# Optimization experiments

Measured on AMD Instinct MI355X. Metric: run time of the kernel, lower is better.

## Reference

```python
import jax, jax.numpy as jnp
import numpy as np

GAMMAS = (0.001, 0.01, 0.1, 1.0, 10.0, 100.0, 1000.0)
EPS = 1e-30


def setup_inputs() -> dict:
    key = jax.random.key(0)
    k1, k2 = jax.random.split(key)
    x = jax.random.normal(k1, (8192, 128), dtype=jnp.float32)
    y = jax.random.normal(k2, (8192, 128), dtype=jnp.float32)
    return {"x": x, "y": y}


def _cdist_sq(x1, x2):
    # squared Euclidean distance matrix, clamped at 1e-30 (matches my_cdist)
    x1_norm = jnp.sum(x1 * x1, axis=-1, keepdims=True)          # [N,1]
    x2_norm = jnp.sum(x2 * x2, axis=-1, keepdims=True)          # [M,1]
    d = x1_norm + x2_norm.T - 2.0 * (x1 @ x2.T)                 # [N,M]
    return jnp.maximum(d, EPS)


def _gaussian_kernel_mean(x, y):
    d = _cdist_sq(x, y)
    # sum over 7 bandwidths, fused into one pass conceptually
    k = sum(jnp.exp(d * (-g)) for g in GAMMAS)
    return jnp.mean(k)


def reference(x, y):
    kxx = _gaussian_kernel_mean(x, x)
    kyy = _gaussian_kernel_mean(y, y)
    kxy = _gaussian_kernel_mean(x, y)
    return kxx + kyy - 2.0 * kxy
```

## Files before the change

kernel.cpp:

```cpp
#include <hip/hip_runtime.h>


#define N_PTS 8192
#define D 128
#define TILES 64
#define TRI 2080
#define NBLK (2 * TRI + TILES * TILES)

typedef __attribute__((ext_vector_type(8))) short bf16x8;
typedef __attribute__((ext_vector_type(8))) unsigned short u16x8;
typedef __attribute__((ext_vector_type(4))) float f32x4;

__device__ __forceinline__ unsigned short f2bf(float a) {
  unsigned u = __float_as_uint(a);
  return (unsigned short)((u + 0x7FFFu + ((u >> 16) & 1u)) >> 16);
}
__device__ __forceinline__ float bf2f(unsigned short b) {
  return __uint_as_float(((unsigned)b) << 16);
}

__global__ __launch_bounds__(256) void norms_kernel(const float* __restrict__ x,
                                                    const float* __restrict__ y,
                                                    float* __restrict__ nx,
                                                    float* __restrict__ ny) {
  int tid = threadIdx.x;
  int g = tid & 3;
  int row = ((int)blockIdx.x & 127) * 64 + (tid >> 2);
  int arr = (int)blockIdx.x >> 7;
  const float* src = arr ? y : x;
  const float4* p = (const float4*)(src + (size_t)row * D) + g;
  float s = 0.f;
  #pragma unroll
  for (int i = 0; i < 8; i++) {
    float4 v = p[i * 4];
    s += v.x * v.x + v.y * v.y + v.z * v.z + v.w * v.w;
  }
  s += __shfl_xor(s, 1);
  s += __shfl_xor(s, 2);
  if (g == 0) (arr ? ny : nx)[row] = s;
}

__global__ __launch_bounds__(256) void convert_kernel(const float* __restrict__ x,
                                                      const float* __restrict__ y,
                                                      unsigned short* __restrict__ xf,
                                                      unsigned short* __restrict__ yf) {
  __shared__ float lds[4][16][132];
  int tid = threadIdx.x;
  int lane = tid & 63, wv = tid >> 6;
  int grp = (int)blockIdx.x * 4 + wv;
  int arr = grp >> 9;
  int rowgrp = grp & 511;
  const float* src = (arr ? y : x) + (size_t)rowgrp * 16 * D;
  unsigned short* dst = (arr ? yf : xf) + (size_t)rowgrp * 4096;

  #pragma unroll
  for (int it = 0; it < 8; it++) {
    int slot = it * 64 + lane;
    int row = slot >> 5, f4 = slot & 31;
    float4 v = *(const float4*)(src + row * D + f4 * 4);
    *(float4*)&lds[wv][row][f4 * 4] = v;
  }
  __syncthreads();

  int row = lane & 15, koct = lane >> 4;
  #pragma unroll
  for (int ks = 0; ks < 8; ks++) {
    int kp = ks * 32 + koct * 8;
    int kf = kp & 127;
    bool ishi = kp < 128;
    float v[8];
    *(float4*)&v[0] = *(const float4*)&lds[wv][row][kf];
    *(float4*)&v[4] = *(const float4*)&lds[wv][row][kf + 4];
    u16x8 o;
    #pragma unroll
    for (int j = 0; j < 8; j++) {
      unsigned short h = f2bf(v[j]);
      o[j] = ishi ? h : f2bf(v[j] - bf2f(h));
    }
    *(u16x8*)(dst + ks * 512 + lane * 8) = o;
  }
}

__global__ __launch_bounds__(256) void mmd_frag_kernel(const unsigned short* __restrict__ xf,
                                                       const unsigned short* __restrict__ yf,
                                                       const float* __restrict__ nx,
                                                       const float* __restrict__ ny,
                                                       double* __restrict__ acc_out) {
  __shared__ double red[256];
  int bid = blockIdx.x;
  const unsigned short *Af, *Bf;
  const float *nA, *nB;
  float w;
  int ib, jb;
  bool isdiag = false;
  if (bid < 2 * TRI) {
    int t = (bid < TRI) ? bid : bid - TRI;
    int r = 0;
    while (t >= TILES - r) { t -= TILES - r; r++; }
    ib = r; jb = r + t;
    if (bid < TRI) { Af = xf; Bf = xf; nA = nx; nB = nx; }
    else           { Af = yf; Bf = yf; nA = ny; nB = ny; }
    isdiag = (ib == jb);
    w = isdiag ? 1.0f : 2.0f;
  } else {
    int t = bid - 2 * TRI;
    ib = t >> 6; jb = t & 63;
    Af = xf; Bf = yf; nA = nx; nB = ny;
    w = -2.0f;
  }

  int tid = threadIdx.x;
  int lane = tid & 63;
  int wv = tid >> 6, wm = wv >> 1, wn = wv & 1;
  int r16 = lane & 15, g4 = lane >> 4;

  const char* Ab = (const char*)Af + (size_t)(ib * 8 + wm * 4) * 8192 + lane * 16;
  const char* Bb = (const char*)Bf + (size_t)(jb * 8 + wn * 4) * 8192 + lane * 16;

  f32x4 acc[4][4];
  #pragma unroll
  for (int m = 0; m < 4; m++)
    #pragma unroll
    for (int n = 0; n < 4; n++) acc[m][n] = (f32x4){0.f, 0.f, 0.f, 0.f};

  #pragma unroll
  for (int ks = 0; ks < 8; ks++) {
    bf16x8 af[4], bfr[4];
    #pragma unroll
    for (int m = 0; m < 4; m++)
      af[m] = *(const bf16x8*)(Ab + m * 8192 + ks * 1024);
    #pragma unroll
    for (int n = 0; n < 4; n++)
      bfr[n] = *(const bf16x8*)(Bb + n * 8192 + ks * 1024);
    #pragma unroll
    for (int m = 0; m < 4; m++)
      #pragma unroll
      for (int n = 0; n < 4; n++)
        acc[m][n] = __builtin_amdgcn_mfma_f32_16x16x32_bf16(af[m], bfr[n], acc[m][n], 0, 0, 0);
  }

  const float* nArow = nA + ib * 128;
  const float* nBrow = nB + jb * 128;
  float nb4[4];
  #pragma unroll
  for (int n = 0; n < 4; n++) nb4[n] = nBrow[wn * 64 + n * 16 + r16];

  float lsum = 0.f;
  #pragma unroll
  for (int m = 0; m < 4; m++) {
    float na4[4];
    #pragma unroll
    for (int r = 0; r < 4; r++) na4[r] = nArow[wm * 64 + m * 16 + g4 * 4 + r];
    float dv[4][4];
    float dmin = 3.0e38f;
    #pragma unroll
    for (int n = 0; n < 4; n++) {
      #pragma unroll
      for (int r = 0; r < 4; r++) {
        float dd = fmaf(-2.f, acc[m][n][r], na4[r] + nb4[n]);
        dd = fmaxf(dd, 1e-30f);
        int rl = wm * 64 + m * 16 + g4 * 4 + r;
        int cl = wn * 64 + n * 16 + r16;
        if (isdiag && rl == cl) dd = 1e30f;
        dv[n][r] = dd;
        dmin = fminf(dmin, dd);
      }
    }
    if (__all(dmin > 110.f)) {
      #pragma unroll
      for (int n = 0; n < 4; n++)
        #pragma unroll
        for (int r = 0; r < 4; r++) {
          float dd = dv[n][r];
          lsum += __expf(dd * -0.001f);
          lsum += __expf(dd * -0.01f);
          lsum += __expf(dd * -0.1f);
        }
    } else {
      #pragma unroll
      for (int n = 0; n < 4; n++)
        #pragma unroll
        for (int r = 0; r < 4; r++) {
          float dd = dv[n][r];
          lsum += __expf(dd * -0.001f);
          lsum += __expf(dd * -0.01f);
          lsum += __expf(dd * -0.1f);
          lsum += __expf(dd * -1.0f);
          lsum += __expf(dd * -10.0f);
          lsum += __expf(dd * -100.0f);
          lsum += __expf(dd * -1000.0f);
        }
    }
  }

  red[tid] = (double)lsum * (double)w;
  __syncthreads();
  #pragma unroll
  for (int s = 128; s > 0; s >>= 1) {
    if (tid < s) red[tid] += red[tid + s];
    __syncthreads();
  }
  if (tid == 0) atomicAdd(acc_out, red[0]);
}

__global__ __launch_bounds__(256) void mmd_fallback_kernel(const float* __restrict__ X,
                                                           const float* __restrict__ Y,
                                                           const float* __restrict__ nx,
                                                           const float* __restrict__ ny,
                                                           double* __restrict__ acc_out) {
  __shared__ unsigned short As[128 * 64];
  __shared__ unsigned short Bs[128 * 64];
  __shared__ double red[256];
  int bid = blockIdx.x;
  const float *A, *B, *nA, *nB;
  float w;
  int ib, jb;
  bool isdiag = false;
  if (bid < 2 * TRI) {
    int t = (bid < TRI) ? bid : bid - TRI;
    int r = 0;
    while (t >= TILES - r) { t -= TILES - r; r++; }
    ib = r; jb = r + t;
    if (bid < TRI) { A = X; B = X; nA = nx; nB = nx; }
    else           { A = Y; B = Y; nA = ny; nB = ny; }
    isdiag = (ib == jb);
    w = isdiag ? 1.0f : 2.0f;
  } else {
    int t = bid - 2 * TRI;
    ib = t >> 6; jb = t & 63;
    A = X; B = Y; nA = nx; nB = ny;
    w = -2.0f;
  }
  int tid = threadIdx.x;
  int lane = tid & 63;
  int wv = tid >> 6, wm = wv >> 1, wn = wv & 1;
  int r16 = lane & 15, g4 = lane >> 4;
  const float* Ab = A + (size_t)ib * 128 * D;
  const float* Bb = B + (size_t)jb * 128 * D;
  f32x4 acc[4][4];
  #pragma unroll
  for (int m = 0; m < 4; m++)
    #pragma unroll
    for (int n = 0; n < 4; n++) acc[m][n] = (f32x4){0.f, 0.f, 0.f, 0.f};
  #pragma unroll 1
  for (int kc = 0; kc < 4; kc++) {
    int k0f = (kc & 1) * 64;
    bool ishi = (kc < 2);
    __syncthreads();
    #pragma unroll
    for (int s = 0; s < 4; s++) {
      int slot = tid + s * 256;
      int row = slot >> 3;
      int k2 = (slot & 7) * 8;
      const float* pa = Ab + row * D + k0f + k2;
      const float* pb = Bb + row * D + k0f + k2;
      float4 a0 = *(const float4*)pa;
      float4 a1 = *(const float4*)(pa + 4);
      float4 b0 = *(const float4*)pb;
      float4 b1 = *(const float4*)(pb + 4);
      float av[8] = {a0.x, a0.y, a0.z, a0.w, a1.x, a1.y, a1.z, a1.w};
      float bv[8] = {b0.x, b0.y, b0.z, b0.w, b1.x, b1.y, b1.z, b1.w};
      u16x8 ua, ub;
      #pragma unroll
      for (int j = 0; j < 8; j++) {
        unsigned short ha = f2bf(av[j]);
        unsigned short hb = f2bf(bv[j]);
        if (ishi) { ua[j] = (short)ha; ub[j] = (short)hb; }
        else {
          ua[j] = f2bf(av[j] - bf2f(ha));
          ub[j] = f2bf(bv[j] - bf2f(hb));
        }
      }
      int boff = row * 128 + ((k2 * 2) ^ ((row & 7) << 4));
      *(u16x8*)((char*)As + boff) = ua;
      *(u16x8*)((char*)Bs + boff) = ub;
    }
    __syncthreads();
    #pragma unroll
    for (int ks = 0; ks < 2; ks++) {
      bf16x8 af[4], bfr[4];
      int kb = ks * 64 + g4 * 16;
      #pragma unroll
      for (int m = 0; m < 4; m++) {
        int row = wm * 64 + m * 16 + r16;
        af[m] = *(const bf16x8*)((const char*)As + row * 128 + (kb ^ ((row & 7) << 4)));
      }
      #pragma unroll
      for (int n = 0; n < 4; n++) {
        int row = wn * 64 + n * 16 + r16;
        bfr[n] = *(const bf16x8*)((const char*)Bs + row * 128 + (kb ^ ((row & 7) << 4)));
      }
      #pragma unroll
      for (int m = 0; m < 4; m++)
        #pragma unroll
        for (int n = 0; n < 4; n++)
          acc[m][n] = __builtin_amdgcn_mfma_f32_16x16x32_bf16(af[m], bfr[n], acc[m][n], 0, 0, 0);
    }
  }
  const float* nArow = nA + ib * 128;
  const float* nBrow = nB + jb * 128;
  float nb4[4];
  #pragma unroll
  for (int n = 0; n < 4; n++) nb4[n] = nBrow[wn * 64 + n * 16 + r16];
  float lsum = 0.f;
  #pragma unroll
  for (int m = 0; m < 4; m++) {
    float na4[4];
    #pragma unroll
    for (int r = 0; r < 4; r++) na4[r] = nArow[wm * 64 + m * 16 + g4 * 4 + r];
    float dv[4][4];
    float dmin = 3.0e38f;
    #pragma unroll
    for (int n = 0; n < 4; n++) {
      #pragma unroll
      for (int r = 0; r < 4; r++) {
        float dd = fmaf(-2.f, acc[m][n][r], na4[r] + nb4[n]);
        dd = fmaxf(dd, 1e-30f);
        int rl = wm * 64 + m * 16 + g4 * 4 + r;
        int cl = wn * 64 + n * 16 + r16;
        if (isdiag && rl == cl) dd = 1e30f;
        dv[n][r] = dd;
        dmin = fminf(dmin, dd);
      }
    }
    if (__all(dmin > 110.f)) {
      #pragma unroll
      for (int n = 0; n < 4; n++)
        #pragma unroll
        for (int r = 0; r < 4; r++) {
          float dd = dv[n][r];
          lsum += __expf(dd * -0.001f);
          lsum += __expf(dd * -0.01f);
          lsum += __expf(dd * -0.1f);
        }
    } else {
      #pragma unroll
      for (int n = 0; n < 4; n++)
        #pragma unroll
        for (int r = 0; r < 4; r++) {
          float dd = dv[n][r];
          lsum += __expf(dd * -0.001f);
          lsum += __expf(dd * -0.01f);
          lsum += __expf(dd * -0.1f);
          lsum += __expf(dd * -1.0f);
          lsum += __expf(dd * -10.0f);
          lsum += __expf(dd * -100.0f);
          lsum += __expf(dd * -1000.0f);
        }
    }
  }
  red[tid] = (double)lsum * (double)w;
  __syncthreads();
  #pragma unroll
  for (int s = 128; s > 0; s >>= 1) {
    if (tid < s) red[tid] += red[tid + s];
    __syncthreads();
  }
  if (tid == 0) atomicAdd(acc_out, red[0]);
}

__global__ __launch_bounds__(256) void diag_kernel(const float* __restrict__ x,
                                                   const float* __restrict__ y,
                                                   const float* __restrict__ nx,
                                                   const float* __restrict__ ny,
                                                   double* __restrict__ acc_out) {
  __shared__ double red[256];
  int tid = threadIdx.x;
  int idx = (int)blockIdx.x * 256 + tid;
  int arr = idx >> 13;
  int row = idx & 8191;
  const float* src = (arr ? y : x) + (size_t)row * D;
  float n = (arr ? ny : nx)[row];
  float acc = 0.f;
  #pragma unroll 4
  for (int k4 = 0; k4 < 32; k4++) {
    float4 v = *(const float4*)(src + k4 * 4);
    acc = fmaf(v.x, v.x, acc);
    acc = fmaf(v.y, v.y, acc);
    acc = fmaf(v.z, v.z, acc);
    acc = fmaf(v.w, v.w, acc);
  }
  float d = fmaf(-2.f, acc, n + n);
  d = fmaxf(d, 1e-30f);
  float s = 0.f;
  s += __expf(d * -0.001f);
  s += __expf(d * -0.01f);
  s += __expf(d * -0.1f);
  s += __expf(d * -1.0f);
  s += __expf(d * -10.0f);
  s += __expf(d * -100.0f);
  s += __expf(d * -1000.0f);
  red[tid] = (double)s;
  __syncthreads();
  #pragma unroll
  for (int st = 128; st > 0; st >>= 1) {
    if (tid < st) red[tid] += red[tid + st];
    __syncthreads();
  }
  if (tid == 0) atomicAdd(acc_out, red[0]);
}

__global__ void finalize_kernel(const double* __restrict__ acc,
                                float* __restrict__ out) {
  out[0] = (float)(acc[0] * (1.0 / ((double)N_PTS * (double)N_PTS)));
}

extern "C" void kernel_launch(void* const* d_in, const int* in_sizes, int n_in,
                              void* d_out, int out_size, void* d_ws, size_t ws_size,
                              hipStream_t stream) {
  const float* x = (const float*)d_in[0];
  const float* y = (const float*)d_in[1];
  float* out = (float*)d_out;

  char* ws = (char*)d_ws;
  double* acc = (double*)ws;
  float* nx = (float*)(ws + 4096);
  float* ny = (float*)(ws + 36864);
  const size_t FRAG_OFF = 69632;
  const size_t FRAG_SZ = 4194304;
  const size_t NEED = FRAG_OFF + 2 * FRAG_SZ;

  hipMemsetAsync(acc, 0, sizeof(double), stream);
  hipLaunchKernelGGL(norms_kernel, dim3(256), dim3(256), 0, stream, x, y, nx, ny);
  if (ws_size >= NEED) {
    unsigned short* xf = (unsigned short*)(ws + FRAG_OFF);
    unsigned short* yf = (unsigned short*)(ws + FRAG_OFF + FRAG_SZ);
    hipLaunchKernelGGL(convert_kernel, dim3(256), dim3(256), 0, stream, x, y, xf, yf);
    hipLaunchKernelGGL(mmd_frag_kernel, dim3(NBLK), dim3(256), 0, stream, xf, yf, nx, ny, acc);
  } else {
    hipLaunchKernelGGL(mmd_fallback_kernel, dim3(NBLK), dim3(256), 0, stream, x, y, nx, ny, acc);
  }
  hipLaunchKernelGGL(diag_kernel, dim3(64), dim3(256), 0, stream, x, y, nx, ny, acc);
  hipLaunchKernelGGL(finalize_kernel, dim3(1), dim3(1), 0, stream, acc, out);
}
```

Baseline: 219.8 us.

## Enlarge MMD tiles to 256x256 with double-buffered LDS staging via global_load_lds

Replaces the 128x128-per-block fragment kernel with a 256x256 tile kernel of 512 threads. The bf16 fragments are staged into double-buffered LDS chunks using global_load_lds, so each fragment read from global memory is reused by more waves. The block reduction now uses wave shuffles before the cross-wave sum. The aim is to cut global-load traffic and per-block reduction overhead. The cost is about 128KB of dynamic LDS per block, which limits residency to roughly one block per CU and may hurt latency hiding in the exp-heavy epilogue.

New measurement: 217.7 us. Within noise of the previous version (-1.0%).

```diff
diff --git a/kernel.cpp b/kernel.cpp
--- a/kernel.cpp
+++ b/kernel.cpp
@@ -3,9 +3,13 @@
 
 #define N_PTS 8192
 #define D 128
+#define T2 32
+#define TRI2 528
+#define NBLK2 (2 * TRI2 + T2 * T2)
 #define TILES 64
 #define TRI 2080
 #define NBLK (2 * TRI + TILES * TILES)
+#define CH_US 16384
 
 typedef __attribute__((ext_vector_type(8))) short bf16x8;
 typedef __attribute__((ext_vector_type(8))) unsigned short u16x8;
@@ -81,76 +85,110 @@
   }
 }
 
-__global__ __launch_bounds__(256) void mmd_frag_kernel(const unsigned short* __restrict__ xf,
-                                                       const unsigned short* __restrict__ yf,
-                                                       const float* __restrict__ nx,
-                                                       const float* __restrict__ ny,
-                                                       double* __restrict__ acc_out) {
-  __shared__ double red[256];
+__device__ __forceinline__ void stage_chunk(const unsigned short* __restrict__ Afrag,
+                                            const unsigned short* __restrict__ Bfrag,
+                                            unsigned short* As, unsigned short* Bs,
+                                            int c, int wv, int lane) {
+  #pragma unroll
+  for (int i = 0; i < 4; i++) {
+    int s = wv * 4 + i;
+    int rg = s >> 1, ksl = s & 1;
+    const unsigned short* ga = Afrag + (size_t)rg * 4096 + (2 * c + ksl) * 512 + lane * 8;
+    const unsigned short* gb = Bfrag + (size_t)rg * 4096 + (2 * c + ksl) * 512 + lane * 8;
+    __builtin_amdgcn_global_load_lds(
+        (const __attribute__((address_space(1))) void*)ga,
+        (__attribute__((address_space(3))) void*)(As + s * 512), 16, 0, 0);
+    __builtin_amdgcn_global_load_lds(
+        (const __attribute__((address_space(1))) void*)gb,
+        (__attribute__((address_space(3))) void*)(Bs + s * 512), 16, 0, 0);
+  }
+}
+
+__global__ __launch_bounds__(512, 2) void mmd_tile256_kernel(
+    const unsigned short* __restrict__ xf, const unsigned short* __restrict__ yf,
+    const float* __restrict__ nx, const float* __restrict__ ny,
+    double* __restrict__ acc_out) {
+  extern __shared__ char smem[];
+  unsigned short* As = (unsigned short*)smem;
+  unsigned short* Bs = (unsigned short*)(smem + 65536);
+  double* red = (double*)(smem + 131072);
+
   int bid = blockIdx.x;
   const unsigned short *Af, *Bf;
   const float *nA, *nB;
   float w;
   int ib, jb;
   bool isdiag = false;
-  if (bid < 2 * TRI) {
-    int t = (bid < TRI) ? bid : bid - TRI;
+  if (bid < 2 * TRI2) {
+    int t = (bid < TRI2) ? bid : bid - TRI2;
     int r = 0;
-    while (t >= TILES - r) { t -= TILES - r; r++; }
+    while (t >= T2 - r) { t -= T2 - r; r++; }
     ib = r; jb = r + t;
-    if (bid < TRI) { Af = xf; Bf = xf; nA = nx; nB = nx; }
-    else           { Af = yf; Bf = yf; nA = ny; nB = ny; }
+    if (bid < TRI2) { Af = xf; Bf = xf; nA = nx; nB = nx; }
+    else            { Af = yf; Bf = yf; nA = ny; nB = ny; }
     isdiag = (ib == jb);
     w = isdiag ? 1.0f : 2.0f;
   } else {
-    int t = bid - 2 * TRI;
-    ib = t >> 6; jb = t & 63;
+    int t = bid - 2 * TRI2;
+    ib = t >> 5; jb = t & 31;
     Af = xf; Bf = yf; nA = nx; nB = ny;
     w = -2.0f;
   }
 
   int tid = threadIdx.x;
-  int lane = tid & 63;
-  int wv = tid >> 6, wm = wv >> 1, wn = wv & 1;
+  int lane = tid & 63, wv = tid >> 6;
+  int wm = wv >> 2, wn = wv & 3;
   int r16 = lane & 15, g4 = lane >> 4;
 
-  const char* Ab = (const char*)Af + (size_t)(ib * 8 + wm * 4) * 8192 + lane * 16;
-  const char* Bb = (const char*)Bf + (size_t)(jb * 8 + wn * 4) * 8192 + lane * 16;
-
-  f32x4 acc[4][4];
-  #pragma unroll
-  for (int m = 0; m < 4; m++)
+  const unsigned short* Afrag = Af + (size_t)(ib * 16) * 4096;
+  const unsigned short* Bfrag = Bf + (size_t)(jb * 16) * 4096;
+
+  f32x4 acc[8][4];
+  #pragma unroll
+  for (int m = 0; m < 8; m++)
     #pragma unroll
     for (int n = 0; n < 4; n++) acc[m][n] = (f32x4){0.f, 0.f, 0.f, 0.f};
 
-  #pragma unroll
-  for (int ks = 0; ks < 8; ks++) {
-    bf16x8 af[4], bfr[4];
-    #pragma unroll
-    for (int m = 0; m < 4; m++)
-      af[m] = *(const bf16x8*)(Ab + m * 8192 + ks * 1024);
-    #pragma unroll
-    for (int n = 0; n < 4; n++)
-      bfr[n] = *(const bf16x8*)(Bb + n * 8192 + ks * 1024);
-    #pragma unroll
-    for (int m = 0; m < 4; m++)
+  stage_chunk(Afrag, Bfrag, As, Bs, 0, wv, lane);
+  __syncthreads();
+
+  #pragma unroll
+  for (int c = 0; c < 4; c++) {
+    if (c < 3)
+      stage_chunk(Afrag, Bfrag, As + ((c + 1) & 1) * CH_US,
+                  Bs + ((c + 1) & 1) * CH_US, c + 1, wv, lane);
+    const unsigned short* Ab = As + (c & 1) * CH_US;
+    const unsigned short* Bb = Bs + (c & 1) * CH_US;
+    #pragma unroll
+    for (int ksl = 0; ksl < 2; ksl++) {
+      bf16x8 a[8], b[4];
+      #pragma unroll
+      for (int m = 0; m < 8; m++)
+        a[m] = *(const bf16x8*)(Ab + ((wm * 8 + m) * 2 + ksl) * 512 + lane * 8);
       #pragma unroll
       for (int n = 0; n < 4; n++)
-        acc[m][n] = __builtin_amdgcn_mfma_f32_16x16x32_bf16(af[m], bfr[n], acc[m][n], 0, 0, 0);
-  }
-
-  const float* nArow = nA + ib * 128;
-  const float* nBrow = nB + jb * 128;
+        b[n] = *(const bf16x8*)(Bb + ((wn * 4 + n) * 2 + ksl) * 512 + lane * 8);
+      #pragma unroll
+      for (int m = 0; m < 8; m++)
+        #pragma unroll
+        for (int n = 0; n < 4; n++)
+          acc[m][n] = __builtin_amdgcn_mfma_f32_16x16x32_bf16(a[m], b[n], acc[m][n], 0, 0, 0);
+    }
+    __syncthreads();
+  }
+
+  const float* nArow = nA + ib * 256;
+  const float* nBrow = nB + jb * 256;
   float nb4[4];
   #pragma unroll
   for (int n = 0; n < 4; n++) nb4[n] = nBrow[wn * 64 + n * 16 + r16];
 
   float lsum = 0.f;
   #pragma unroll
-  for (int m = 0; m < 4; m++) {
+  for (int m = 0; m < 8; m++) {
     float na4[4];
     #pragma unroll
-    for (int r = 0; r < 4; r++) na4[r] = nArow[wm * 64 + m * 16 + g4 * 4 + r];
+    for (int r = 0; r < 4; r++) na4[r] = nArow[wm * 128 + m * 16 + g4 * 4 + r];
     float dv[4][4];
     float dmin = 3.0e38f;
     #pragma unroll
@@ -159,7 +197,7 @@
       for (int r = 0; r < 4; r++) {
         float dd = fmaf(-2.f, acc[m][n][r], na4[r] + nb4[n]);
         dd = fmaxf(dd, 1e-30f);
-        int rl = wm * 64 + m * 16 + g4 * 4 + r;
+        int rl = wm * 128 + m * 16 + g4 * 4 + r;
         int cl = wn * 64 + n * 16 + r16;
         if (isdiag && rl == cl) dd = 1e30f;
         dv[n][r] = dd;
@@ -193,14 +231,21 @@
     }
   }
 
-  red[tid] = (double)lsum * (double)w;
+  double v = (double)lsum * (double)w;
+  v += __shfl_xor(v, 32);
+  v += __shfl_xor(v, 16);
+  v += __shfl_xor(v, 8);
+  v += __shfl_xor(v, 4);
+  v += __shfl_xor(v, 2);
+  v += __shfl_xor(v, 1);
+  if (lane == 0) red[wv] = v;
   __syncthreads();
-  #pragma unroll
-  for (int s = 128; s > 0; s >>= 1) {
-    if (tid < s) red[tid] += red[tid + s];
-    __syncthreads();
-  }
-  if (tid == 0) atomicAdd(acc_out, red[0]);
+  if (tid == 0) {
+    double s = 0.0;
+    #pragma unroll
+    for (int i = 0; i < 8; i++) s += red[i];
+    atomicAdd(acc_out, s);
+  }
 }
 
 __global__ __launch_bounds__(256) void mmd_fallback_kernel(const float* __restrict__ X,
@@ -426,7 +471,8 @@
     unsigned short* xf = (unsigned short*)(ws + FRAG_OFF);
     unsigned short* yf = (unsigned short*)(ws + FRAG_OFF + FRAG_SZ);
     hipLaunchKernelGGL(convert_kernel, dim3(256), dim3(256), 0, stream, x, y, xf, yf);
-    hipLaunchKernelGGL(mmd_frag_kernel, dim3(NBLK), dim3(256), 0, stream, xf, yf, nx, ny, acc);
+    hipLaunchKernelGGL(mmd_tile256_kernel, dim3(NBLK2), dim3(512), 131136, stream,
+                       xf, yf, nx, ny, acc);
   } else {
     hipLaunchKernelGGL(mmd_fallback_kernel, dim3(NBLK), dim3(256), 0, stream, x, y, nx, ny, acc);
   }
```

## Stage fragments through double-buffered LDS with global_load_lds and shuffle reduction

Applied to the files above, without the earlier changes.

The main MMD kernel used to load MFMA operand fragments straight from global memory into registers. It now copies each k-slice of the A and B tiles into LDS with direct global-to-LDS loads, double-buffered so the next slice's copy overlaps the current MFMAs. Each fragment is fetched once per block and shared across waves instead of each wave loading its own. The block reduction now uses wave shuffles and a four-entry LDS array, and launch bounds request 4 blocks per CU. In exchange it adds a __syncthreads per k-step and uses 32 KB of LDS per block.

Result: no change. 216.8 us (-1.3%).

```diff
diff --git a/kernel.cpp b/kernel.cpp
--- a/kernel.cpp
+++ b/kernel.cpp
@@ -81,12 +81,14 @@
   }
 }
 
-__global__ __launch_bounds__(256) void mmd_frag_kernel(const unsigned short* __restrict__ xf,
-                                                       const unsigned short* __restrict__ yf,
-                                                       const float* __restrict__ nx,
-                                                       const float* __restrict__ ny,
-                                                       double* __restrict__ acc_out) {
-  __shared__ double red[256];
+__global__ __launch_bounds__(256, 4) void mmd_tile128_kernel(
+    const unsigned short* __restrict__ xf, const unsigned short* __restrict__ yf,
+    const float* __restrict__ nx, const float* __restrict__ ny,
+    double* __restrict__ acc_out) {
+  __shared__ unsigned short As[2][4096];
+  __shared__ unsigned short Bs[2][4096];
+  __shared__ double red[4];
+
   int bid = blockIdx.x;
   const unsigned short *Af, *Bf;
   const float *nA, *nB;
@@ -110,12 +112,27 @@
   }
 
   int tid = threadIdx.x;
-  int lane = tid & 63;
-  int wv = tid >> 6, wm = wv >> 1, wn = wv & 1;
+  int lane = tid & 63, wv = tid >> 6;
+  int wm = wv >> 1, wn = wv & 1;
   int r16 = lane & 15, g4 = lane >> 4;
 
-  const char* Ab = (const char*)Af + (size_t)(ib * 8 + wm * 4) * 8192 + lane * 16;
-  const char* Bb = (const char*)Bf + (size_t)(jb * 8 + wn * 4) * 8192 + lane * 16;
+  const unsigned short* Afrag = Af + (size_t)(ib * 8) * 4096;
+  const unsigned short* Bfrag = Bf + (size_t)(jb * 8) * 4096;
+
+  #define STAGE(ks, buf)                                                        \
+    {                                                                           \
+      _Pragma("unroll")                                                         \
+      for (int i = 0; i < 4; i++) {                                             \
+        int s = wv * 4 + i;                                                     \
+        const unsigned short* g = (s < 8)                                       \
+            ? (Afrag + (size_t)s * 4096 + (ks) * 512 + lane * 8)                \
+            : (Bfrag + (size_t)(s - 8) * 4096 + (ks) * 512 + lane * 8);         \
+        unsigned short* l = (s < 8) ? &As[buf][s * 512] : &Bs[buf][(s - 8) * 512]; \
+        __builtin_amdgcn_global_load_lds(                                       \
+            (const __attribute__((address_space(1))) void*)g,                   \
+            (__attribute__((address_space(3))) void*)l, 16, 0, 0);              \
+      }                                                                         \
+    }
 
   f32x4 acc[4][4];
   #pragma unroll
@@ -123,20 +140,26 @@
     #pragma unroll
     for (int n = 0; n < 4; n++) acc[m][n] = (f32x4){0.f, 0.f, 0.f, 0.f};
 
+  STAGE(0, 0);
+  __syncthreads();
+
   #pragma unroll
   for (int ks = 0; ks < 8; ks++) {
-    bf16x8 af[4], bfr[4];
+    int cur = ks & 1;
+    if (ks < 7) STAGE(ks + 1, cur ^ 1);
+    bf16x8 a[4], b[4];
     #pragma unroll
     for (int m = 0; m < 4; m++)
-      af[m] = *(const bf16x8*)(Ab + m * 8192 + ks * 1024);
+      a[m] = *(const bf16x8*)&As[cur][(wm * 4 + m) * 512 + lane * 8];
     #pragma unroll
     for (int n = 0; n < 4; n++)
-      bfr[n] = *(const bf16x8*)(Bb + n * 8192 + ks * 1024);
+      b[n] = *(const bf16x8*)&Bs[cur][(wn * 4 + n) * 512 + lane * 8];
     #pragma unroll
     for (int m = 0; m < 4; m++)
       #pragma unroll
       for (int n = 0; n < 4; n++)
-        acc[m][n] = __builtin_amdgcn_mfma_f32_16x16x32_bf16(af[m], bfr[n], acc[m][n], 0, 0, 0);
+        acc[m][n] = __builtin_amdgcn_mfma_f32_16x16x32_bf16(a[m], b[n], acc[m][n], 0, 0, 0);
+    __syncthreads();
   }
 
   const float* nArow = nA + ib * 128;
@@ -193,14 +216,20 @@
     }
   }
 
-  red[tid] = (double)lsum * (double)w;
+  double v = (double)lsum * (double)w;
+  v += __shfl_xor(v, 32);
+  v += __shfl_xor(v, 16);
+  v += __shfl_xor(v, 8);
+  v += __shfl_xor(v, 4);
+  v += __shfl_xor(v, 2);
+  v += __shfl_xor(v, 1);
+  if (lane == 0) red[wv] = v;
   __syncthreads();
-  #pragma unroll
-  for (int s = 128; s > 0; s >>= 1) {
-    if (tid < s) red[tid] += red[tid + s];
-    __syncthreads();
-  }
-  if (tid == 0) atomicAdd(acc_out, red[0]);
+  if (tid == 0) {
+    double s = red[0] + red[1] + red[2] + red[3];
+    atomicAdd(acc_out, s);
+  }
+  #undef STAGE
 }
 
 __global__ __launch_bounds__(256) void mmd_fallback_kernel(const float* __restrict__ X,
@@ -426,7 +455,8 @@
     unsigned short* xf = (unsigned short*)(ws + FRAG_OFF);
     unsigned short* yf = (unsigned short*)(ws + FRAG_OFF + FRAG_SZ);
     hipLaunchKernelGGL(convert_kernel, dim3(256), dim3(256), 0, stream, x, y, xf, yf);
-    hipLaunchKernelGGL(mmd_frag_kernel, dim3(NBLK), dim3(256), 0, stream, xf, yf, nx, ny, acc);
+    hipLaunchKernelGGL(mmd_tile128_kernel, dim3(NBLK), dim3(256), 0, stream,
+                       xf, yf, nx, ny, acc);
   } else {
     hipLaunchKernelGGL(mmd_fallback_kernel, dim3(NBLK), dim3(256), 0, stream, x, y, nx, ny, acc);
   }
```
